# Kernel optimization log

Measured on AMD Instinct MI355X. Metric: run time of the kernel, lower is better.

Reference implementation:

```python
import jax, jax.numpy as jnp
import numpy as np

N, E, F_IN, F_E, HID, HEADS = 20000, 320000, 256, 32, 128, 4
NEG_SLOPE = 0.2  # PyG GATConv default negative_slope


def _segment_softmax(logits, seg, num_segments):
    # logits: [E, H] softmax over edges sharing the same destination node
    m = jax.ops.segment_max(logits, seg, num_segments=num_segments)
    m = jnp.where(jnp.isfinite(m), m, 0.0)
    e = jnp.exp(logits - m[seg])
    s = jax.ops.segment_sum(e, seg, num_segments=num_segments)
    return e / s[seg]


def _gat_layer(x, edge_attr, src, dst, W, We, a_src, a_dst, a_edge, bias, num_nodes):
    H, C = a_src.shape
    h = (x @ W).reshape(-1, H, C)            # [N, H, C]
    he = (edge_attr @ We).reshape(-1, H, C)  # [E, H, C]
    alpha = (h * a_src).sum(-1)[src] + (h * a_dst).sum(-1)[dst] + (he * a_edge).sum(-1)
    alpha = jax.nn.leaky_relu(alpha, NEG_SLOPE)          # [E, H]
    alpha = _segment_softmax(alpha, dst, num_nodes)
    out = jax.ops.segment_sum(h[src] * alpha[..., None], dst, num_segments=num_nodes)
    return out.reshape(num_nodes, H * C) + bias


def setup_inputs() -> dict:
    key = jax.random.key(0)
    ks = jax.random.split(key, 20)
    s1 = 1.0 / np.sqrt(F_IN)
    s2 = 1.0 / np.sqrt(HID * HEADS)
    se = 1.0 / np.sqrt(F_E)
    sh = 1.0 / np.sqrt(HID)
    return {
        "x": jax.random.normal(ks[0], (N, F_IN), jnp.float32),
        "edge_index": jax.random.randint(ks[1], (2, E), 0, N),
        "edge_attr": jax.random.normal(ks[2], (E, F_E), jnp.float32),
        # GAT layer 1: in=F_IN, heads=HEADS, out=HID, concat=True
        "W1": jax.random.normal(ks[3], (F_IN, HEADS * HID), jnp.float32) * s1,
        "We1": jax.random.normal(ks[4], (F_E, HEADS * HID), jnp.float32) * se,
        "as1": jax.random.normal(ks[5], (HEADS, HID), jnp.float32) * sh,
        "ad1": jax.random.normal(ks[6], (HEADS, HID), jnp.float32) * sh,
        "ae1": jax.random.normal(ks[7], (HEADS, HID), jnp.float32) * sh,
        "b1": jnp.zeros((HEADS * HID,), jnp.float32),
        # GAT layer 2: in=HEADS*HID, heads=1, out=HID
        "W2": jax.random.normal(ks[8], (HEADS * HID, HID), jnp.float32) * s2,
        "We2": jax.random.normal(ks[9], (F_E, HID), jnp.float32) * se,
        "as2": jax.random.normal(ks[10], (1, HID), jnp.float32) * sh,
        "ad2": jax.random.normal(ks[11], (1, HID), jnp.float32) * sh,
        "ae2": jax.random.normal(ks[12], (1, HID), jnp.float32) * sh,
        "b2": jnp.zeros((HID,), jnp.float32),
        # projection head: Linear(HID,HID) -> PReLU -> Linear(HID,HID)
        "P1": jax.random.normal(ks[13], (HID, HID), jnp.float32) * sh,
        "pb1": jnp.zeros((HID,), jnp.float32),
        "prelu_a": jnp.float32(0.25),
        "P2": jax.random.normal(ks[14], (HID, HID), jnp.float32) * sh,
        "pb2": jnp.zeros((HID,), jnp.float32),
    }


def reference(x, edge_index, edge_attr, W1, We1, as1, ad1, ae1, b1,
              W2, We2, as2, ad2, ae2, b2, P1, pb1, prelu_a, P2, pb2):
    # eval mode: edge dropout / feature dropout are no-ops
    ei = jnp.concatenate([edge_index, edge_index[::-1]], axis=1)  # add reversed edges
    ea = jnp.concatenate([edge_attr, edge_attr], axis=0)
    src, dst = ei[0], ei[1]
    n = x.shape[0]
    h = jax.nn.elu(_gat_layer(x, ea, src, dst, W1, We1, as1, ad1, ae1, b1, n))
    h = jax.nn.elu(_gat_layer(h, ea, src, dst, W2, We2, as2, ad2, ae2, b2, n))
    z = h @ P1 + pb1
    z = jnp.where(z > 0, z, prelu_a * z)  # PReLU (single shared parameter)
    h_proj = z @ P2 + pb2
    g = jax.nn.sigmoid(h_proj.mean(axis=0))
    return h_proj, g
```

## Files before the change

### kernel.cpp

```cpp
#include <hip/hip_runtime.h>
#include <hip/hip_bf16.h>


#define NN    20000
#define EE    320000
#define E2    640000
#define FIN   256
#define FE    32
#define HIDD  128
#define NHEAD 4
#define HH    512
#define CAP   160
#define AW    132

typedef unsigned short ushort_t;
typedef short frag8 __attribute__((ext_vector_type(8)));
typedef float f32x4 __attribute__((ext_vector_type(4)));

__device__ inline ushort_t f2bf(float f){
  unsigned x = __float_as_uint(f);
  unsigned r = (x + 0x7fffu + ((x>>16)&1u)) >> 16;
  return (ushort_t)r;
}
__device__ inline float bf2f(ushort_t u){ return __uint_as_float(((unsigned)u)<<16); }
__device__ inline float lo_of(unsigned v){ return __uint_as_float(v<<16); }
__device__ inline float hi_of(unsigned v){ return __uint_as_float(v & 0xffff0000u); }

__global__ void prep(const int* __restrict__ ei, int* __restrict__ cnt,
                     const float* __restrict__ x, ushort_t* __restrict__ xb,
                     const float* __restrict__ W1, ushort_t* __restrict__ W1t,
                     const float* __restrict__ W2, ushort_t* __restrict__ W2t,
                     const float* __restrict__ P1, ushort_t* __restrict__ P1th, ushort_t* __restrict__ P1tl,
                     const float* __restrict__ P2, ushort_t* __restrict__ P2th, ushort_t* __restrict__ P2tl,
                     const float* __restrict__ We1, const float* __restrict__ ae1,
                     const float* __restrict__ We2, const float* __restrict__ ae2,
                     float* __restrict__ v1, float* __restrict__ v2){
  int b = blockIdx.x, tid = threadIdx.x;
  if(b < 2500){
    int e = b*256 + tid;
    int dst = (e < EE) ? ei[EE + e] : ei[e - EE];
    atomicAdd(&cnt[dst], 1);
  } else if(b < 7500){
    int i = (b-2500)*256 + tid;
    float4 v = ((const float4*)x)[i];
    ushort4 o; o.x=f2bf(v.x); o.y=f2bf(v.y); o.z=f2bf(v.z); o.w=f2bf(v.w);
    ((ushort4*)xb)[i] = o;
  } else if(b < 8012){
    int idx = (b-7500)*256 + tid;
    int k = idx>>9, n = idx&511;
    W1t[n*FIN + k] = f2bf(W1[idx]);
  } else if(b < 8268){
    int idx = (b-8012)*256 + tid;
    int k = idx>>7, n = idx&127;
    W2t[n*HH + k] = f2bf(W2[idx]);
  } else if(b < 8332){
    int idx = (b-8268)*256 + tid;
    int k = idx>>7, n = idx&127;
    float v = P1[idx];
    ushort_t h = f2bf(v);
    P1th[n*HIDD + k] = h;
    P1tl[n*HIDD + k] = f2bf(v - bf2f(h));
  } else if(b < 8396){
    int idx = (b-8332)*256 + tid;
    int k = idx>>7, n = idx&127;
    float v = P2[idx];
    ushort_t h = f2bf(v);
    P2th[n*HIDD + k] = h;
    P2tl[n*HIDD + k] = f2bf(v - bf2f(h));
  } else {
    if(tid < FE*NHEAD){
      int f = tid>>2, h = tid&3;
      float s = 0.f;
      for(int c=0;c<HIDD;c++) s += We1[f*HH + h*HIDD + c] * ae1[h*HIDD + c];
      v1[f*4+h] = s;
    } else if(tid < FE*NHEAD + FE){
      int f = tid - FE*NHEAD;
      float s = 0.f;
      for(int c=0;c<HIDD;c++) s += We2[f*HIDD + c] * ae2[c];
      v2[f] = s;
    }
  }
}

__global__ void scan_k(const int* __restrict__ cnt, int* __restrict__ rowptr){
  __shared__ int sums[1024];
  int tid = threadIdx.x;
  const int per = 20;
  int base = tid*per;
  int v[20];
  if(base + per <= NN){
    #pragma unroll
    for(int q=0;q<5;q++) *(int4*)&v[q*4] = *(const int4*)&cnt[base + q*4];
  } else {
    for(int i=0;i<per;i++) v[i] = (base+i<NN)? cnt[base+i] : 0;
  }
  int s = 0;
  #pragma unroll
  for(int i=0;i<per;i++) s += v[i];
  sums[tid] = s; __syncthreads();
  for(int off=1; off<1024; off<<=1){
    int t = (tid>=off)? sums[tid-off] : 0;
    __syncthreads();
    sums[tid] += t;
    __syncthreads();
  }
  int run = (tid==0)? 0 : sums[tid-1];
  int rp[20];
  #pragma unroll
  for(int i=0;i<per;i++){ rp[i] = run; run += v[i]; }
  if(base + per <= NN){
    #pragma unroll
    for(int q=0;q<5;q++) *(int4*)&rowptr[base + q*4] = *(const int4*)&rp[q*4];
  } else {
    for(int i=0;i<per;i++) if(base+i<=NN) rowptr[base+i] = rp[i];
  }
  if(base == NN) rowptr[NN] = rp[0];
  if(tid == 1023 && base + per == NN) rowptr[NN] = run;
  if(tid == 1000) rowptr[NN] = rp[0];
}

__global__ __launch_bounds__(256) void csr_gemm1(
    const int* __restrict__ ei, const float* __restrict__ ea,
    const float* __restrict__ v1, const float* __restrict__ v2,
    const int* __restrict__ rowptr, int* __restrict__ fcnt,
    int* __restrict__ csrc, float* __restrict__ cae1, float* __restrict__ cae2,
    const ushort_t* __restrict__ A, const ushort_t* __restrict__ Bt,
    ushort_t* __restrict__ C, int M,
    const float* __restrict__ as1, const float* __restrict__ ad1,
    float* __restrict__ s1n, float* __restrict__ d1n){
  __shared__ ushort_t As[128*32];
  __shared__ ushort_t Bs[128*32];
  __shared__ float sred[2][128], dred[2][128];
  __shared__ float sv1[FE*NHEAD];
  __shared__ float sv2[FE];
  int tid = threadIdx.x;
  int b = blockIdx.x;
  if(b < 1250){
    if(tid < FE*NHEAD) sv1[tid] = v1[tid];
    if(tid < FE)       sv2[tid] = v2[tid];
    __syncthreads();
    int e = b*256 + tid;
    int a = ei[e], bb = ei[EE+e];
    const float4* er4 = (const float4*)(ea + (long)e*FE);
    float a0=0,a1=0,a2=0,a3=0,ab=0;
    #pragma unroll
    for(int f4=0; f4<FE/4; f4++){
      float4 t = er4[f4];
      float tv[4] = {t.x, t.y, t.z, t.w};
      #pragma unroll
      for(int c=0;c<4;c++){
        int f = f4*4+c;
        float t1 = tv[c];
        a0 += t1*sv1[f*4+0]; a1 += t1*sv1[f*4+1]; a2 += t1*sv1[f*4+2]; a3 += t1*sv1[f*4+3];
        ab += t1*sv2[f];
      }
    }
    float4 c4; c4.x=a0; c4.y=a1; c4.z=a2; c4.w=a3;
    int pos = rowptr[bb] + atomicAdd(&fcnt[bb], 1);
    csrc[pos] = a;
    *(float4*)(cae1 + (size_t)pos*4) = c4;
    cae2[pos] = ab;
    pos = rowptr[a] + atomicAdd(&fcnt[a], 1);
    csrc[pos] = bb;
    *(float4*)(cae1 + (size_t)pos*4) = c4;
    cae2[pos] = ab;
    return;
  }
  int g = b - 1250;
  int head = g & 3;
  int m0 = (g>>2)*128, n0 = head*128;
  int w = tid>>6, lane = tid&63;
  int qr = (w>>1)*64, qc = (w&1)*64;
  int lrow = lane&15, koff = (lane>>4)*8;
  f32x4 acc[4][4] = {};
  for(int k0=0; k0<FIN; k0+=32){
    #pragma unroll
    for(int rep=0;rep<2;rep++){
      int segid = tid + rep*256;
      int row = segid>>2, off = (segid&3)*8;
      int gr = m0 + row;
      int4 va = (gr<M) ? *(const int4*)(A + (long)gr*FIN + k0 + off) : int4{0,0,0,0};
      *(int4*)&As[row*32 + off] = va;
      int4 vb = *(const int4*)(Bt + (long)(n0+row)*FIN + k0 + off);
      *(int4*)&Bs[row*32 + off] = vb;
    }
    __syncthreads();
    frag8 af[4], bfr[4];
    #pragma unroll
    for(int i=0;i<4;i++) af[i]  = *(const frag8*)&As[(qr + i*16 + lrow)*32 + koff];
    #pragma unroll
    for(int j=0;j<4;j++) bfr[j] = *(const frag8*)&Bs[(qc + j*16 + lrow)*32 + koff];
    #pragma unroll
    for(int i=0;i<4;i++)
      #pragma unroll
      for(int j=0;j<4;j++)
        acc[i][j] = __builtin_amdgcn_mfma_f32_16x16x32_bf16(af[i], bfr[j], acc[i][j], 0,0,0);
    __syncthreads();
  }
  #pragma unroll
  for(int i=0;i<4;i++)
    #pragma unroll
    for(int j=0;j<4;j++)
      #pragma unroll
      for(int r=0;r<4;r++){
        int row = m0 + qr + i*16 + (lane>>4)*4 + r;
        int col = n0 + qc + j*16 + (lane&15);
        if(row<M) C[(long)row*HH + col] = f2bf(acc[i][j][r]);
      }
  float a_s[4], a_d[4];
  #pragma unroll
  for(int j=0;j<4;j++){
    a_s[j] = as1[head*HIDD + qc + j*16 + (lane&15)];
    a_d[j] = ad1[head*HIDD + qc + j*16 + (lane&15)];
  }
  #pragma unroll
  for(int i=0;i<4;i++)
    #pragma unroll
    for(int r=0;r<4;r++){
      float sp = acc[i][0][r]*a_s[0] + acc[i][1][r]*a_s[1] + acc[i][2][r]*a_s[2] + acc[i][3][r]*a_s[3];
      float dp = acc[i][0][r]*a_d[0] + acc[i][1][r]*a_d[1] + acc[i][2][r]*a_d[2] + acc[i][3][r]*a_d[3];
      #pragma unroll
      for(int o=1;o<=8;o<<=1){ sp += __shfl_xor(sp,o,64); dp += __shfl_xor(dp,o,64); }
      if((lane&15)==0){
        int rl = qr + i*16 + (lane>>4)*4 + r;
        sred[w&1][rl] = sp;
        dred[w&1][rl] = dp;
      }
    }
  __syncthreads();
  if(tid < 128){
    int gr = m0 + tid;
    if(gr < M){
      s1n[gr*4 + head] = sred[0][tid] + sred[1][tid];
      d1n[gr*4 + head] = dred[0][tid] + dred[1][tid];
    }
  }
}

__global__ __launch_bounds__(256) void gemm64_attn(const ushort_t* __restrict__ A, const ushort_t* __restrict__ Bt,
                                                   ushort_t* __restrict__ C, int M,
                                                   const float* __restrict__ as2, const float* __restrict__ ad2,
                                                   float* __restrict__ s2n, float* __restrict__ d2n){
  __shared__ ushort_t As[64*32];
  __shared__ ushort_t Bs[128*32];
  __shared__ float sred[4][64], dred[4][64];
  int tid = threadIdx.x;
  int m0 = blockIdx.y*64;
  int w = tid>>6, lane = tid&63;
  int qc = w*32;
  int lrow = lane&15, koff = (lane>>4)*8;
  f32x4 acc[4][2] = {};
  for(int k0=0; k0<HH; k0+=32){
    {
      int row = tid>>2, off = (tid&3)*8;
      int gr = m0 + row;
      int4 va = (gr<M) ? *(const int4*)(A + (long)gr*HH + k0 + off) : int4{0,0,0,0};
      *(int4*)&As[row*32 + off] = va;
    }
    #pragma unroll
    for(int rep=0;rep<2;rep++){
      int segid = tid + rep*256;
      int row = segid>>2, off = (segid&3)*8;
      int4 vb = *(const int4*)(Bt + (long)row*HH + k0 + off);
      *(int4*)&Bs[row*32 + off] = vb;
    }
    __syncthreads();
    frag8 af[4], bfr[2];
    #pragma unroll
    for(int i=0;i<4;i++) af[i]  = *(const frag8*)&As[(i*16 + lrow)*32 + koff];
    #pragma unroll
    for(int j=0;j<2;j++) bfr[j] = *(const frag8*)&Bs[(qc + j*16 + lrow)*32 + koff];
    #pragma unroll
    for(int i=0;i<4;i++)
      #pragma unroll
      for(int j=0;j<2;j++)
        acc[i][j] = __builtin_amdgcn_mfma_f32_16x16x32_bf16(af[i], bfr[j], acc[i][j], 0,0,0);
    __syncthreads();
  }
  #pragma unroll
  for(int i=0;i<4;i++)
    #pragma unroll
    for(int j=0;j<2;j++)
      #pragma unroll
      for(int r=0;r<4;r++){
        int row = m0 + i*16 + (lane>>4)*4 + r;
        int col = qc + j*16 + (lane&15);
        if(row<M) C[(long)row*HIDD + col] = f2bf(acc[i][j][r]);
      }
  float a_s[2], a_d[2];
  #pragma unroll
  for(int j=0;j<2;j++){
    a_s[j] = as2[qc + j*16 + (lane&15)];
    a_d[j] = ad2[qc + j*16 + (lane&15)];
  }
  #pragma unroll
  for(int i=0;i<4;i++)
    #pragma unroll
    for(int r=0;r<4;r++){
      float sp = acc[i][0][r]*a_s[0] + acc[i][1][r]*a_s[1];
      float dp = acc[i][0][r]*a_d[0] + acc[i][1][r]*a_d[1];
      #pragma unroll
      for(int o=1;o<=8;o<<=1){ sp += __shfl_xor(sp,o,64); dp += __shfl_xor(dp,o,64); }
      if((lane&15)==0){
        int rl = i*16 + (lane>>4)*4 + r;
        sred[w][rl] = sp;
        dred[w][rl] = dp;
      }
    }
  __syncthreads();
  if(tid < 64){
    int gr = m0 + tid;
    if(gr < M){
      s2n[gr] = sred[0][tid]+sred[1][tid]+sred[2][tid]+sred[3][tid];
      d2n[gr] = dred[0][tid]+dred[1][tid]+dred[2][tid]+dred[3][tid];
    }
  }
}

__global__ __launch_bounds__(256) void agg1(const ushort_t* __restrict__ h1b, const int* __restrict__ rowptr,
                     const int* __restrict__ csrc,
                     const float* __restrict__ s1n, const float* __restrict__ d1n,
                     const float* __restrict__ cae1,
                     const float* __restrict__ b1, ushort_t* __restrict__ out1b){
  __shared__ float stw[2][CAP*4];
  __shared__ int   sidx[2][CAP];
  __shared__ float pm[2][2][4], ps[2][2][4];
  int tid = threadIdx.x;
  int nodeLoc = tid>>7;
  int wv2 = (tid>>6)&1;
  int lane = tid&63;
  int n = blockIdx.x*2 + nodeLoc;
  int beg = rowptr[n], end = rowptr[n+1];
  int deg = end - beg;
  int h12 = lane&3;
  float dh = d1n[n*4 + h12];
  float m = -1e30f, ss = 0.f;
  for(int base=beg + wv2*16; base<end; base+=32){
    int e = base + (lane>>2);
    if(e<end){
      int s = csrc[e];
      float t = s1n[s*4 + h12] + dh + cae1[e*4 + h12];
      t = t>0.f? t : 0.2f*t;
      int j = e - beg;
      if(j < CAP){
        stw[nodeLoc][j*4 + h12] = t;
        if(h12==0) sidx[nodeLoc][j] = s;
      }
      float nm = fmaxf(m, t);
      ss = ss*__expf(m-nm) + __expf(t-nm);
      m = nm;
    }
  }
  #pragma unroll
  for(int o=4;o<=32;o<<=1){
    float mo = __shfl_xor(m, o, 64), so = __shfl_xor(ss, o, 64);
    float nm = fmaxf(m, mo);
    ss = ss*__expf(m-nm) + so*__expf(mo-nm);
    m = nm;
  }
  if(lane<4){ pm[nodeLoc][wv2][lane] = m; ps[nodeLoc][wv2][lane] = ss; }
  __syncthreads();
  float m4[4], i4[4];
  #pragma unroll
  for(int h=0;h<4;h++){
    float mA = pm[nodeLoc][0][h], mB = pm[nodeLoc][1][h];
    float sA = ps[nodeLoc][0][h], sB = ps[nodeLoc][1][h];
    float mf = fmaxf(mA, mB);
    float sf = sA*__expf(mA-mf) + sB*__expf(mB-mf);
    m4[h] = mf; i4[h] = sf>0.f ? 1.f/sf : 0.f;
  }
  int capn = deg < CAP ? deg : CAP;
  int tln = tid & 127;
  float mh = m4[h12], ih = i4[h12];
  for(int f=tln; f<capn*4; f+=128) stw[nodeLoc][f] = __expf(stw[nodeLoc][f]-mh)*ih;
  __syncthreads();
  int hq = wv2*2 + (lane>>5);
  long cOff = (long)(wv2*256 + lane*4);
  float acc0=0.f, acc1=0.f, acc2=0.f, acc3=0.f;
  int j = 0;
  for(; j+3<capn; j+=4){
    int s0 = sidx[nodeLoc][j],   s1 = sidx[nodeLoc][j+1];
    int s2 = sidx[nodeLoc][j+2], s3 = sidx[nodeLoc][j+3];
    float w0 = stw[nodeLoc][(j  )*4 + hq];
    float w1 = stw[nodeLoc][(j+1)*4 + hq];
    float w2 = stw[nodeLoc][(j+2)*4 + hq];
    float w3 = stw[nodeLoc][(j+3)*4 + hq];
    uint2 v0 = *(const uint2*)(h1b + (long)s0*HH + cOff);
    uint2 v1 = *(const uint2*)(h1b + (long)s1*HH + cOff);
    uint2 v2 = *(const uint2*)(h1b + (long)s2*HH + cOff);
    uint2 v3 = *(const uint2*)(h1b + (long)s3*HH + cOff);
    acc0 += w0*lo_of(v0.x) + w1*lo_of(v1.x) + w2*lo_of(v2.x) + w3*lo_of(v3.x);
    acc1 += w0*hi_of(v0.x) + w1*hi_of(v1.x) + w2*hi_of(v2.x) + w3*hi_of(v3.x);
    acc2 += w0*lo_of(v0.y) + w1*lo_of(v1.y) + w2*lo_of(v2.y) + w3*lo_of(v3.y);
    acc3 += w0*hi_of(v0.y) + w1*hi_of(v1.y) + w2*hi_of(v2.y) + w3*hi_of(v3.y);
  }
  for(; j<capn; j++){
    int s0 = sidx[nodeLoc][j];
    float w0 = stw[nodeLoc][j*4 + hq];
    uint2 v0 = *(const uint2*)(h1b + (long)s0*HH + cOff);
    acc0 += w0*lo_of(v0.x); acc1 += w0*hi_of(v0.x);
    acc2 += w0*lo_of(v0.y); acc3 += w0*hi_of(v0.y);
  }
  for(; j<deg; j++){
    int e = beg + j;
    int s0 = csrc[e];
    float t = s1n[s0*4 + hq] + d1n[n*4 + hq] + cae1[e*4 + hq];
    t = t>0.f? t : 0.2f*t;
    float w0 = __expf(t - m4[hq])*i4[hq];
    uint2 v0 = *(const uint2*)(h1b + (long)s0*HH + cOff);
    acc0 += w0*lo_of(v0.x); acc1 += w0*hi_of(v0.x);
    acc2 += w0*lo_of(v0.y); acc3 += w0*hi_of(v0.y);
  }
  float4 bb = *(const float4*)(b1 + cOff);
  float o0 = acc0 + bb.x, o1 = acc1 + bb.y, o2 = acc2 + bb.z, o3 = acc3 + bb.w;
  o0 = o0>0.f? o0 : __expf(o0)-1.f;
  o1 = o1>0.f? o1 : __expf(o1)-1.f;
  o2 = o2>0.f? o2 : __expf(o2)-1.f;
  o3 = o3>0.f? o3 : __expf(o3)-1.f;
  uint2 pk;
  pk.x = (unsigned)f2bf(o0) | ((unsigned)f2bf(o1)<<16);
  pk.y = (unsigned)f2bf(o2) | ((unsigned)f2bf(o3)<<16);
  *(uint2*)(out1b + (long)n*HH + cOff) = pk;
}

__global__ __launch_bounds__(256) void agg2(const ushort_t* __restrict__ h2b, const int* __restrict__ rowptr,
                     const int* __restrict__ csrc,
                     const float* __restrict__ s2n, const float* __restrict__ d2n,
                     const float* __restrict__ cae2,
                     const float* __restrict__ b2, float* __restrict__ out2){
  __shared__ float stl[4][CAP];
  __shared__ int   sid[4][CAP];
  int tid = threadIdx.x;
  int wv = tid>>6, lane = tid&63;
  int n = blockIdx.x*4 + wv;
  int beg = rowptr[n], end = rowptr[n+1];
  int deg = end - beg;
  float dn = d2n[n];
  float m = -1e30f, ss = 0.f;
  for(int e=beg+lane; e<end; e+=64){
    int s = csrc[e];
    float t = s2n[s] + dn + cae2[e];
    t = t>0.f? t : 0.2f*t;
    int j = e - beg;
    if(j < CAP){ stl[wv][j] = t; sid[wv][j] = s; }
    float nm = fmaxf(m, t);
    ss = ss*__expf(m-nm) + __expf(t-nm);
    m = nm;
  }
  #pragma unroll
  for(int o=1;o<=32;o<<=1){
    float mo = __shfl_xor(m, o, 64), so = __shfl_xor(ss, o, 64);
    float nm = fmaxf(m, mo);
    ss = ss*__expf(m-nm) + so*__expf(mo-nm);
    m = nm;
  }
  float inv = ss>0.f ? 1.f/ss : 0.f;
  int capn = deg < CAP ? deg : CAP;
  for(int j=lane; j<capn; j+=64) stl[wv][j] = __expf(stl[wv][j]-m)*inv;
  float a0=0.f, a1=0.f;
  int j = 0;
  for(; j+3<capn; j+=4){
    int s0 = sid[wv][j], s1 = sid[wv][j+1], s2 = sid[wv][j+2], s3 = sid[wv][j+3];
    float w0 = stl[wv][j], w1 = stl[wv][j+1], w2 = stl[wv][j+2], w3 = stl[wv][j+3];
    unsigned v0 = *(const unsigned*)(h2b + (long)s0*HIDD + 2*lane);
    unsigned v1 = *(const unsigned*)(h2b + (long)s1*HIDD + 2*lane);
    unsigned v2 = *(const unsigned*)(h2b + (long)s2*HIDD + 2*lane);
    unsigned v3 = *(const unsigned*)(h2b + (long)s3*HIDD + 2*lane);
    a0 += w0*lo_of(v0) + w1*lo_of(v1) + w2*lo_of(v2) + w3*lo_of(v3);
    a1 += w0*hi_of(v0) + w1*hi_of(v1) + w2*hi_of(v2) + w3*hi_of(v3);
  }
  for(; j<capn; j++){
    float w0 = stl[wv][j];
    unsigned v0 = *(const unsigned*)(h2b + (long)sid[wv][j]*HIDD + 2*lane);
    a0 += w0*lo_of(v0); a1 += w0*hi_of(v0);
  }
  for(; j<deg; j++){
    int e = beg + j;
    int s0 = csrc[e];
    float t = s2n[s0] + dn + cae2[e];
    t = t>0.f? t : 0.2f*t;
    float w0 = __expf(t-m)*inv;
    unsigned v0 = *(const unsigned*)(h2b + (long)s0*HIDD + 2*lane);
    a0 += w0*lo_of(v0); a1 += w0*hi_of(v0);
  }
  float o0 = a0 + b2[2*lane];
  float o1 = a1 + b2[2*lane+1];
  float2 pk;
  pk.x = o0>0.f? o0 : __expf(o0)-1.f;
  pk.y = o1>0.f? o1 : __expf(o1)-1.f;
  *(float2*)(out2 + (long)n*HIDD + 2*lane) = pk;
}

__global__ __launch_bounds__(256) void proj_fused(const float* __restrict__ A,
    const ushort_t* __restrict__ P1th, const ushort_t* __restrict__ P1tl,
    const ushort_t* __restrict__ P2th, const ushort_t* __restrict__ P2tl,
    const float* __restrict__ pb1, const float* __restrict__ pra,
    const float* __restrict__ pb2, float* __restrict__ OUT, int M,
    float* __restrict__ gbuf){
  __shared__ ushort_t Ah[64*AW], Al[64*AW];
  __shared__ ushort_t Bh[128*32], Bl[128*32];
  int tid = threadIdx.x;
  int m0 = blockIdx.x*64;
  int w = tid>>6, lane = tid&63;
  int qc = w*32;
  int lrow = lane&15, koff2 = (lane>>4)*8;
  f32x4 acc[4][2] = {};
  {
    int row = tid>>2, cb = (tid&3)*8;
    int gr = m0 + row;
    for(int c0=0;c0<HIDD;c0+=32){
      float4 u0{0,0,0,0}, u1{0,0,0,0};
      if(gr<M){
        u0 = *(const float4*)(A + (long)gr*HIDD + c0 + cb);
        u1 = *(const float4*)(A + (long)gr*HIDD + c0 + cb + 4);
      }
      float vv[8] = {u0.x,u0.y,u0.z,u0.w,u1.x,u1.y,u1.z,u1.w};
      unsigned ph[4], pl[4];
      #pragma unroll
      for(int c=0;c<4;c++){
        ushort_t h0 = f2bf(vv[2*c]),   l0 = f2bf(vv[2*c]   - bf2f(h0));
        ushort_t h1 = f2bf(vv[2*c+1]), l1 = f2bf(vv[2*c+1] - bf2f(h1));
        ph[c] = (unsigned)h0 | ((unsigned)h1<<16);
        pl[c] = (unsigned)l0 | ((unsigned)l1<<16);
      }
      *(uint4*)&Ah[row*AW + c0 + cb] = *(uint4*)ph;
      *(uint4*)&Al[row*AW + c0 + cb] = *(uint4*)pl;
    }
  }
  __syncthreads();
  for(int k0=0;k0<HIDD;k0+=32){
    #pragma unroll
    for(int rep=0;rep<2;rep++){
      int segid = tid + rep*256;
      int row = segid>>2, off = (segid&3)*8;
      *(int4*)&Bh[row*32 + off] = *(const int4*)(P1th + (long)row*HIDD + k0 + off);
      *(int4*)&Bl[row*32 + off] = *(const int4*)(P1tl + (long)row*HIDD + k0 + off);
    }
    __syncthreads();
    frag8 afh[4], afl[4], bfh[2], bfl[2];
    #pragma unroll
    for(int i=0;i<4;i++){
      afh[i] = *(const frag8*)&Ah[(i*16 + lrow)*AW + k0 + koff2];
      afl[i] = *(const frag8*)&Al[(i*16 + lrow)*AW + k0 + koff2];
    }
    #pragma unroll
    for(int j=0;j<2;j++){
      bfh[j] = *(const frag8*)&Bh[(qc + j*16 + lrow)*32 + koff2];
      bfl[j] = *(const frag8*)&Bl[(qc + j*16 + lrow)*32 + koff2];
    }
    #pragma unroll
    for(int i=0;i<4;i++)
      #pragma unroll
      for(int j=0;j<2;j++){
        acc[i][j] = __builtin_amdgcn_mfma_f32_16x16x32_bf16(afh[i], bfh[j], acc[i][j], 0,0,0);
        acc[i][j] = __builtin_amdgcn_mfma_f32_16x16x32_bf16(afh[i], bfl[j], acc[i][j], 0,0,0);
        acc[i][j] = __builtin_amdgcn_mfma_f32_16x16x32_bf16(afl[i], bfh[j], acc[i][j], 0,0,0);
      }
    __syncthreads();
  }
  float ap = pra[0];
  #pragma unroll
  for(int i=0;i<4;i++)
    #pragma unroll
    for(int j=0;j<2;j++)
      #pragma unroll
      for(int r=0;r<4;r++){
        int row = i*16 + (lane>>4)*4 + r;
        int col = qc + j*16 + (lane&15);
        float v = acc[i][j][r] + pb1[col];
        v = v>0.f? v : ap*v;
        ushort_t h = f2bf(v);
        Ah[row*AW + col] = h;
        Al[row*AW + col] = f2bf(v - bf2f(h));
        acc[i][j][r] = 0.f;
      }
  __syncthreads();
  for(int k0=0;k0<HIDD;k0+=32){
    #pragma unroll
    for(int rep=0;rep<2;rep++){
      int segid = tid + rep*256;
      int row = segid>>2, off = (segid&3)*8;
      *(int4*)&Bh[row*32 + off] = *(const int4*)(P2th + (long)row*HIDD + k0 + off);
      *(int4*)&Bl[row*32 + off] = *(const int4*)(P2tl + (long)row*HIDD + k0 + off);
    }
    __syncthreads();
    frag8 afh[4], afl[4], bfh[2], bfl[2];
    #pragma unroll
    for(int i=0;i<4;i++){
      afh[i] = *(const frag8*)&Ah[(i*16 + lrow)*AW + k0 + koff2];
      afl[i] = *(const frag8*)&Al[(i*16 + lrow)*AW + k0 + koff2];
    }
    #pragma unroll
    for(int j=0;j<2;j++){
      bfh[j] = *(const frag8*)&Bh[(qc + j*16 + lrow)*32 + koff2];
      bfl[j] = *(const frag8*)&Bl[(qc + j*16 + lrow)*32 + koff2];
    }
    #pragma unroll
    for(int i=0;i<4;i++)
      #pragma unroll
      for(int j=0;j<2;j++){
        acc[i][j] = __builtin_amdgcn_mfma_f32_16x16x32_bf16(afh[i], bfh[j], acc[i][j], 0,0,0);
        acc[i][j] = __builtin_amdgcn_mfma_f32_16x16x32_bf16(afh[i], bfl[j], acc[i][j], 0,0,0);
        acc[i][j] = __builtin_amdgcn_mfma_f32_16x16x32_bf16(afl[i], bfh[j], acc[i][j], 0,0,0);
      }
    __syncthreads();
  }
  float cs[2] = {0.f, 0.f};
  #pragma unroll
  for(int i=0;i<4;i++)
    #pragma unroll
    for(int j=0;j<2;j++)
      #pragma unroll
      for(int r=0;r<4;r++){
        int rowg = m0 + i*16 + (lane>>4)*4 + r;
        int col = qc + j*16 + (lane&15);
        if(rowg<M){
          float v = acc[i][j][r] + pb2[col];
          OUT[(long)rowg*HIDD + col] = v;
          cs[j] += v;
        }
      }
  #pragma unroll
  for(int j=0;j<2;j++){
    cs[j] += __shfl_xor(cs[j],16,64);
    cs[j] += __shfl_xor(cs[j],32,64);
    if((lane>>4)==0) atomicAdd(&gbuf[qc + j*16 + (lane&15)], cs[j]);
  }
}

__global__ void sigmoid_g(const float* __restrict__ gbuf, float* __restrict__ gout){
  int c = threadIdx.x;
  float m = gbuf[c] * (1.0f/NN);
  gout[c] = 1.f/(1.f+__expf(-m));
}


extern "C" void kernel_launch(void* const* d_in, const int* in_sizes, int n_in,
                              void* d_out, int out_size, void* d_ws, size_t ws_size,
                              hipStream_t stream){
  const float* x    = (const float*)d_in[0];
  const int*   ei   = (const int*)  d_in[1];
  const float* ea   = (const float*)d_in[2];
  const float* W1   = (const float*)d_in[3];
  const float* We1  = (const float*)d_in[4];
  const float* as1  = (const float*)d_in[5];
  const float* ad1  = (const float*)d_in[6];
  const float* ae1  = (const float*)d_in[7];
  const float* b1   = (const float*)d_in[8];
  const float* W2   = (const float*)d_in[9];
  const float* We2  = (const float*)d_in[10];
  const float* as2  = (const float*)d_in[11];
  const float* ad2  = (const float*)d_in[12];
  const float* ae2  = (const float*)d_in[13];
  const float* b2   = (const float*)d_in[14];
  const float* P1   = (const float*)d_in[15];
  const float* pb1  = (const float*)d_in[16];
  const float* pra  = (const float*)d_in[17];
  const float* P2   = (const float*)d_in[18];
  const float* pb2  = (const float*)d_in[19];
  float* out = (float*)d_out;

  char* wsp = (char*)d_ws;
  size_t off = 0;
  auto alloc = [&](size_t bytes)->char*{
    char* p = wsp + off;
    off += (bytes + 255) & ~(size_t)255;
    return p;
  };
  ushort_t* h1b  = (ushort_t*)alloc(sizeof(ushort_t)*(size_t)NN*HH);
  ushort_t* out1b= (ushort_t*)alloc(sizeof(ushort_t)*(size_t)NN*HH);
  ushort_t* h2b  = (ushort_t*)alloc(sizeof(ushort_t)*(size_t)NN*HIDD);
  float*    out2 = (float*)  alloc(sizeof(float)*(size_t)NN*HIDD);
  ushort_t* xb   = (ushort_t*)alloc(sizeof(ushort_t)*(size_t)NN*FIN);
  ushort_t* W1t  = (ushort_t*)alloc(sizeof(ushort_t)*(size_t)HH*FIN);
  ushort_t* W2t  = (ushort_t*)alloc(sizeof(ushort_t)*(size_t)HIDD*HH);
  ushort_t* P1th = (ushort_t*)alloc(sizeof(ushort_t)*(size_t)HIDD*HIDD);
  ushort_t* P1tl = (ushort_t*)alloc(sizeof(ushort_t)*(size_t)HIDD*HIDD);
  ushort_t* P2th = (ushort_t*)alloc(sizeof(ushort_t)*(size_t)HIDD*HIDD);
  ushort_t* P2tl = (ushort_t*)alloc(sizeof(ushort_t)*(size_t)HIDD*HIDD);
  float* s1n   = (float*)alloc(sizeof(float)*NN*NHEAD);
  float* d1n   = (float*)alloc(sizeof(float)*NN*NHEAD);
  float* s2n   = (float*)alloc(sizeof(float)*NN);
  float* d2n   = (float*)alloc(sizeof(float)*NN);
  float* v1    = (float*)alloc(sizeof(float)*FE*NHEAD);
  float* v2    = (float*)alloc(sizeof(float)*FE);
  float* cae1  = (float*)alloc(sizeof(float)*(size_t)E2*NHEAD);
  float* cae2  = (float*)alloc(sizeof(float)*(size_t)E2);
  int*   rowptr= (int*)  alloc(sizeof(int)*(NN+1));
  int*   csrc  = (int*)  alloc(sizeof(int)*(size_t)E2);
  int*   cnt   = (int*)  alloc(sizeof(int)*NN);
  int*   fcnt  = (int*)  alloc(sizeof(int)*NN);
  float* gbuf  = (float*)alloc(sizeof(float)*HIDD);

  hipMemsetAsync(cnt, 0, 80128 + 80128 + 512, stream);

  prep     <<<8397, 256, 0, stream>>>(ei, cnt, x, xb, W1, W1t, W2, W2t,
                                      P1, P1th, P1tl, P2, P2th, P2tl,
                                      We1, ae1, We2, ae2, v1, v2);
  scan_k   <<<1, 1024, 0, stream>>>(cnt, rowptr);
  csr_gemm1<<<1250 + 628, 256, 0, stream>>>(ei, ea, v1, v2, rowptr, fcnt, csrc, cae1, cae2,
                                            xb, W1t, h1b, NN, as1, ad1, s1n, d1n);
  agg1     <<<NN/2, 256, 0, stream>>>(h1b, rowptr, csrc, s1n, d1n, cae1, b1, out1b);
  gemm64_attn<<<dim3(1, (NN+63)/64), 256, 0, stream>>>(out1b, W2t, h2b, NN, as2, ad2, s2n, d2n);
  agg2     <<<NN/4, 256, 0, stream>>>(h2b, rowptr, csrc, s2n, d2n, cae2, b2, out2);
  proj_fused<<<(NN+63)/64, 256, 0, stream>>>(out2, P1th, P1tl, P2th, P2tl,
                                             pb1, pra, pb2, out, NN, gbuf);
  sigmoid_g<<<1, 128, 0, stream>>>(gbuf, out + (size_t)NN*HIDD);
}
```

Before: 373.4 us.

## Split edge range across two waves per node in both aggregation kernels

```diff
diff --git a/kernel.cpp b/kernel.cpp
--- a/kernel.cpp
+++ b/kernel.cpp
@@ -114,8 +114,6 @@
   } else {
     for(int i=0;i<per;i++) if(base+i<=NN) rowptr[base+i] = rp[i];
   }
-  if(base == NN) rowptr[NN] = rp[0];
-  if(tid == 1023 && base + per == NN) rowptr[NN] = run;
   if(tid == 1000) rowptr[NN] = rp[0];
 }
 
@@ -325,9 +323,10 @@
   __shared__ float stw[2][CAP*4];
   __shared__ int   sidx[2][CAP];
   __shared__ float pm[2][2][4], ps[2][2][4];
+  __shared__ float part[2][8][64];
   int tid = threadIdx.x;
   int nodeLoc = tid>>7;
-  int wv2 = (tid>>6)&1;
+  int wv = (tid>>6)&1;
   int lane = tid&63;
   int n = blockIdx.x*2 + nodeLoc;
   int beg = rowptr[n], end = rowptr[n+1];
@@ -335,7 +334,7 @@
   int h12 = lane&3;
   float dh = d1n[n*4 + h12];
   float m = -1e30f, ss = 0.f;
-  for(int base=beg + wv2*16; base<end; base+=32){
+  for(int base=beg + wv*16; base<end; base+=32){
     int e = base + (lane>>2);
     if(e<end){
       int s = csrc[e];
@@ -358,7 +357,7 @@
     ss = ss*__expf(m-nm) + so*__expf(mo-nm);
     m = nm;
   }
-  if(lane<4){ pm[nodeLoc][wv2][lane] = m; ps[nodeLoc][wv2][lane] = ss; }
+  if(lane<4){ pm[nodeLoc][wv][lane] = m; ps[nodeLoc][wv][lane] = ss; }
   __syncthreads();
   float m4[4], i4[4];
   #pragma unroll
@@ -374,53 +373,77 @@
   float mh = m4[h12], ih = i4[h12];
   for(int f=tln; f<capn*4; f+=128) stw[nodeLoc][f] = __expf(stw[nodeLoc][f]-mh)*ih;
   __syncthreads();
-  int hq = wv2*2 + (lane>>5);
-  long cOff = (long)(wv2*256 + lane*4);
-  float acc0=0.f, acc1=0.f, acc2=0.f, acc3=0.f;
-  int j = 0;
-  for(; j+3<capn; j+=4){
+  int hq = lane>>4;
+  int half = (capn+1)>>1;
+  int gb = wv*half;
+  int ge = (gb+half < capn) ? gb+half : capn;
+  float acc[8] = {};
+  int j = gb;
+  for(; j+3<ge; j+=4){
     int s0 = sidx[nodeLoc][j],   s1 = sidx[nodeLoc][j+1];
     int s2 = sidx[nodeLoc][j+2], s3 = sidx[nodeLoc][j+3];
     float w0 = stw[nodeLoc][(j  )*4 + hq];
     float w1 = stw[nodeLoc][(j+1)*4 + hq];
     float w2 = stw[nodeLoc][(j+2)*4 + hq];
     float w3 = stw[nodeLoc][(j+3)*4 + hq];
-    uint2 v0 = *(const uint2*)(h1b + (long)s0*HH + cOff);
-    uint2 v1 = *(const uint2*)(h1b + (long)s1*HH + cOff);
-    uint2 v2 = *(const uint2*)(h1b + (long)s2*HH + cOff);
-    uint2 v3 = *(const uint2*)(h1b + (long)s3*HH + cOff);
-    acc0 += w0*lo_of(v0.x) + w1*lo_of(v1.x) + w2*lo_of(v2.x) + w3*lo_of(v3.x);
-    acc1 += w0*hi_of(v0.x) + w1*hi_of(v1.x) + w2*hi_of(v2.x) + w3*hi_of(v3.x);
-    acc2 += w0*lo_of(v0.y) + w1*lo_of(v1.y) + w2*lo_of(v2.y) + w3*lo_of(v3.y);
-    acc3 += w0*hi_of(v0.y) + w1*hi_of(v1.y) + w2*hi_of(v2.y) + w3*hi_of(v3.y);
-  }
-  for(; j<capn; j++){
+    uint4 v0 = *(const uint4*)(h1b + (long)s0*HH + lane*8);
+    uint4 v1 = *(const uint4*)(h1b + (long)s1*HH + lane*8);
+    uint4 v2 = *(const uint4*)(h1b + (long)s2*HH + lane*8);
+    uint4 v3 = *(const uint4*)(h1b + (long)s3*HH + lane*8);
+    acc[0] += w0*lo_of(v0.x) + w1*lo_of(v1.x) + w2*lo_of(v2.x) + w3*lo_of(v3.x);
+    acc[1] += w0*hi_of(v0.x) + w1*hi_of(v1.x) + w2*hi_of(v2.x) + w3*hi_of(v3.x);
+    acc[2] += w0*lo_of(v0.y) + w1*lo_of(v1.y) + w2*lo_of(v2.y) + w3*lo_of(v3.y);
+    acc[3] += w0*hi_of(v0.y) + w1*hi_of(v1.y) + w2*hi_of(v2.y) + w3*hi_of(v3.y);
+    acc[4] += w0*lo_of(v0.z) + w1*lo_of(v1.z) + w2*lo_of(v2.z) + w3*lo_of(v3.z);
+    acc[5] += w0*hi_of(v0.z) + w1*hi_of(v1.z) + w2*hi_of(v2.z) + w3*hi_of(v3.z);
+    acc[6] += w0*lo_of(v0.w) + w1*lo_of(v1.w) + w2*lo_of(v2.w) + w3*lo_of(v3.w);
+    acc[7] += w0*hi_of(v0.w) + w1*hi_of(v1.w) + w2*hi_of(v2.w) + w3*hi_of(v3.w);
+  }
+  for(; j<ge; j++){
     int s0 = sidx[nodeLoc][j];
     float w0 = stw[nodeLoc][j*4 + hq];
-    uint2 v0 = *(const uint2*)(h1b + (long)s0*HH + cOff);
-    acc0 += w0*lo_of(v0.x); acc1 += w0*hi_of(v0.x);
-    acc2 += w0*lo_of(v0.y); acc3 += w0*hi_of(v0.y);
-  }
-  for(; j<deg; j++){
-    int e = beg + j;
+    uint4 v0 = *(const uint4*)(h1b + (long)s0*HH + lane*8);
+    acc[0] += w0*lo_of(v0.x); acc[1] += w0*hi_of(v0.x);
+    acc[2] += w0*lo_of(v0.y); acc[3] += w0*hi_of(v0.y);
+    acc[4] += w0*lo_of(v0.z); acc[5] += w0*hi_of(v0.z);
+    acc[6] += w0*lo_of(v0.w); acc[7] += w0*hi_of(v0.w);
+  }
+  for(int jj=CAP+wv; jj<deg; jj+=2){
+    int e = beg + jj;
     int s0 = csrc[e];
     float t = s1n[s0*4 + hq] + d1n[n*4 + hq] + cae1[e*4 + hq];
     t = t>0.f? t : 0.2f*t;
     float w0 = __expf(t - m4[hq])*i4[hq];
-    uint2 v0 = *(const uint2*)(h1b + (long)s0*HH + cOff);
-    acc0 += w0*lo_of(v0.x); acc1 += w0*hi_of(v0.x);
-    acc2 += w0*lo_of(v0.y); acc3 += w0*hi_of(v0.y);
-  }
-  float4 bb = *(const float4*)(b1 + cOff);
-  float o0 = acc0 + bb.x, o1 = acc1 + bb.y, o2 = acc2 + bb.z, o3 = acc3 + bb.w;
-  o0 = o0>0.f? o0 : __expf(o0)-1.f;
-  o1 = o1>0.f? o1 : __expf(o1)-1.f;
-  o2 = o2>0.f? o2 : __expf(o2)-1.f;
-  o3 = o3>0.f? o3 : __expf(o3)-1.f;
-  uint2 pk;
-  pk.x = (unsigned)f2bf(o0) | ((unsigned)f2bf(o1)<<16);
-  pk.y = (unsigned)f2bf(o2) | ((unsigned)f2bf(o3)<<16);
-  *(uint2*)(out1b + (long)n*HH + cOff) = pk;
+    uint4 v0 = *(const uint4*)(h1b + (long)s0*HH + lane*8);
+    acc[0] += w0*lo_of(v0.x); acc[1] += w0*hi_of(v0.x);
+    acc[2] += w0*lo_of(v0.y); acc[3] += w0*hi_of(v0.y);
+    acc[4] += w0*lo_of(v0.z); acc[5] += w0*hi_of(v0.z);
+    acc[6] += w0*lo_of(v0.w); acc[7] += w0*hi_of(v0.w);
+  }
+  if(wv==1){
+    #pragma unroll
+    for(int c=0;c<8;c++) part[nodeLoc][c][lane] = acc[c];
+  }
+  __syncthreads();
+  if(wv==0){
+    #pragma unroll
+    for(int c=0;c<8;c++) acc[c] += part[nodeLoc][c][lane];
+    float4 bl = ((const float4*)b1)[lane*2];
+    float4 bh = ((const float4*)b1)[lane*2+1];
+    float bb[8] = {bl.x,bl.y,bl.z,bl.w,bh.x,bh.y,bh.z,bh.w};
+    ushort_t o8[8];
+    #pragma unroll
+    for(int c=0;c<8;c++){
+      float o = acc[c] + bb[c];
+      o8[c] = f2bf(o>0.f? o : __expf(o)-1.f);
+    }
+    uint4 pk;
+    pk.x = (unsigned)o8[0] | ((unsigned)o8[1]<<16);
+    pk.y = (unsigned)o8[2] | ((unsigned)o8[3]<<16);
+    pk.z = (unsigned)o8[4] | ((unsigned)o8[5]<<16);
+    pk.w = (unsigned)o8[6] | ((unsigned)o8[7]<<16);
+    *(uint4*)(out1b + (long)n*HH + lane*8) = pk;
+  }
 }
 
 __global__ __launch_bounds__(256) void agg2(const ushort_t* __restrict__ h2b, const int* __restrict__ rowptr,
@@ -428,21 +451,25 @@
                      const float* __restrict__ s2n, const float* __restrict__ d2n,
                      const float* __restrict__ cae2,
                      const float* __restrict__ b2, float* __restrict__ out2){
-  __shared__ float stl[4][CAP];
-  __shared__ int   sid[4][CAP];
+  __shared__ float stl[2][CAP];
+  __shared__ int   sid[2][CAP];
+  __shared__ float pm2[2][2], ps2[2][2];
+  __shared__ float part2[2][2][64];
   int tid = threadIdx.x;
-  int wv = tid>>6, lane = tid&63;
-  int n = blockIdx.x*4 + wv;
+  int nodeLoc = tid>>7;
+  int wv = (tid>>6)&1;
+  int lane = tid&63;
+  int n = blockIdx.x*2 + nodeLoc;
   int beg = rowptr[n], end = rowptr[n+1];
   int deg = end - beg;
   float dn = d2n[n];
   float m = -1e30f, ss = 0.f;
-  for(int e=beg+lane; e<end; e+=64){
+  for(int e=beg + wv*64 + lane; e<end; e+=128){
     int s = csrc[e];
     float t = s2n[s] + dn + cae2[e];
     t = t>0.f? t : 0.2f*t;
     int j = e - beg;
-    if(j < CAP){ stl[wv][j] = t; sid[wv][j] = s; }
+    if(j < CAP){ stl[nodeLoc][j] = t; sid[nodeLoc][j] = s; }
     float nm = fmaxf(m, t);
     ss = ss*__expf(m-nm) + __expf(t-nm);
     m = nm;
@@ -454,14 +481,26 @@
     ss = ss*__expf(m-nm) + so*__expf(mo-nm);
     m = nm;
   }
+  if(lane==0){ pm2[nodeLoc][wv] = m; ps2[nodeLoc][wv] = ss; }
+  __syncthreads();
+  {
+    float mA = pm2[nodeLoc][0], mB = pm2[nodeLoc][1];
+    float sA = ps2[nodeLoc][0], sB = ps2[nodeLoc][1];
+    m = fmaxf(mA, mB);
+    ss = sA*__expf(mA-m) + sB*__expf(mB-m);
+  }
   float inv = ss>0.f ? 1.f/ss : 0.f;
   int capn = deg < CAP ? deg : CAP;
-  for(int j=lane; j<capn; j+=64) stl[wv][j] = __expf(stl[wv][j]-m)*inv;
+  for(int j=tid&127; j<capn; j+=128) stl[nodeLoc][j] = __expf(stl[nodeLoc][j]-m)*inv;
+  __syncthreads();
+  int half = (capn+1)>>1;
+  int gb = wv*half;
+  int ge = (gb+half < capn) ? gb+half : capn;
   float a0=0.f, a1=0.f;
-  int j = 0;
-  for(; j+3<capn; j+=4){
-    int s0 = sid[wv][j], s1 = sid[wv][j+1], s2 = sid[wv][j+2], s3 = sid[wv][j+3];
-    float w0 = stl[wv][j], w1 = stl[wv][j+1], w2 = stl[wv][j+2], w3 = stl[wv][j+3];
+  int j = gb;
+  for(; j+3<ge; j+=4){
+    int s0 = sid[nodeLoc][j], s1 = sid[nodeLoc][j+1], s2 = sid[nodeLoc][j+2], s3 = sid[nodeLoc][j+3];
+    float w0 = stl[nodeLoc][j], w1 = stl[nodeLoc][j+1], w2 = stl[nodeLoc][j+2], w3 = stl[nodeLoc][j+3];
     unsigned v0 = *(const unsigned*)(h2b + (long)s0*HIDD + 2*lane);
     unsigned v1 = *(const unsigned*)(h2b + (long)s1*HIDD + 2*lane);
     unsigned v2 = *(const unsigned*)(h2b + (long)s2*HIDD + 2*lane);
@@ -469,13 +508,13 @@
     a0 += w0*lo_of(v0) + w1*lo_of(v1) + w2*lo_of(v2) + w3*lo_of(v3);
     a1 += w0*hi_of(v0) + w1*hi_of(v1) + w2*hi_of(v2) + w3*hi_of(v3);
   }
-  for(; j<capn; j++){
-    float w0 = stl[wv][j];
-    unsigned v0 = *(const unsigned*)(h2b + (long)sid[wv][j]*HIDD + 2*lane);
+  for(; j<ge; j++){
+    float w0 = stl[nodeLoc][j];
+    unsigned v0 = *(const unsigned*)(h2b + (long)sid[nodeLoc][j]*HIDD + 2*lane);
     a0 += w0*lo_of(v0); a1 += w0*hi_of(v0);
   }
-  for(; j<deg; j++){
-    int e = beg + j;
+  for(int jj=CAP+wv; jj<deg; jj+=2){
+    int e = beg + jj;
     int s0 = csrc[e];
     float t = s2n[s0] + dn + cae2[e];
     t = t>0.f? t : 0.2f*t;
@@ -483,12 +522,21 @@
     unsigned v0 = *(const unsigned*)(h2b + (long)s0*HIDD + 2*lane);
     a0 += w0*lo_of(v0); a1 += w0*hi_of(v0);
   }
-  float o0 = a0 + b2[2*lane];
-  float o1 = a1 + b2[2*lane+1];
-  float2 pk;
-  pk.x = o0>0.f? o0 : __expf(o0)-1.f;
-  pk.y = o1>0.f? o1 : __expf(o1)-1.f;
-  *(float2*)(out2 + (long)n*HIDD + 2*lane) = pk;
+  if(wv==1){
+    part2[nodeLoc][0][lane] = a0;
+    part2[nodeLoc][1][lane] = a1;
+  }
+  __syncthreads();
+  if(wv==0){
+    a0 += part2[nodeLoc][0][lane];
+    a1 += part2[nodeLoc][1][lane];
+    float o0 = a0 + b2[2*lane];
+    float o1 = a1 + b2[2*lane+1];
+    float2 pk;
+    pk.x = o0>0.f? o0 : __expf(o0)-1.f;
+    pk.y = o1>0.f? o1 : __expf(o1)-1.f;
+    *(float2*)(out2 + (long)n*HIDD + 2*lane) = pk;
+  }
 }
 
 __global__ __launch_bounds__(256) void proj_fused(const float* __restrict__ A,
@@ -702,7 +750,7 @@
                                             xb, W1t, h1b, NN, as1, ad1, s1n, d1n);
   agg1     <<<NN/2, 256, 0, stream>>>(h1b, rowptr, csrc, s1n, d1n, cae1, b1, out1b);
   gemm64_attn<<<dim3(1, (NN+63)/64), 256, 0, stream>>>(out1b, W2t, h2b, NN, as2, ad2, s2n, d2n);
-  agg2     <<<NN/4, 256, 0, stream>>>(h2b, rowptr, csrc, s2n, d2n, cae2, b2, out2);
+  agg2     <<<NN/2, 256, 0, stream>>>(h2b, rowptr, csrc, s2n, d2n, cae2, b2, out2);
   proj_fused<<<(NN+63)/64, 256, 0, stream>>>(out2, P1th, P1tl, P2th, P2tl,
                                              pb1, pra, pb2, out, NN, gbuf);
   sigmoid_g<<<1, 128, 0, stream>>>(gbuf, out + (size_t)NN*HIDD);
```

After: 381.4 us. +2.1%, slower.
